# Performance work log

Hardware: AMD Instinct MI355X
Metric: run time of the kernel (lower is better)

Reference implementation:

```python
import jax, jax.numpy as jnp
import numpy as np

VOL = 64          # self.vol_size
SPACE = 0.2       # space_size (cubic), space_center = 0
IMG = 255.0       # normalization constant in the source (2*u/255 - 1)


def setup_inputs() -> dict:
    key = jax.random.key(0)
    ks = jax.random.split(key, 5)
    B, V, C, Hf, Wf = 2, 4, 32, 64, 64
    features = jax.random.normal(ks[0], (B, V, C, Hf, Wf), jnp.float32)
    # near-identity rotations, cameras ~0.5m away, focal ~200, principal point 128
    camera_R = jnp.eye(3, dtype=jnp.float32)[None, None] + 0.01 * jax.random.normal(ks[1], (B, V, 3, 3), jnp.float32)
    camera_T = jnp.array([0.0, 0.0, 0.5], jnp.float32) + 0.01 * jax.random.normal(ks[2], (B, V, 3), jnp.float32)
    K0 = jnp.array([[200.0, 0.0, 128.0], [0.0, 200.0, 128.0], [0.0, 0.0, 1.0]], jnp.float32)
    Kmask = jnp.array([[1.0, 0.0, 1.0], [0.0, 1.0, 1.0], [0.0, 0.0, 0.0]], jnp.float32)
    camera_K = K0[None, None] + 0.5 * jax.random.normal(ks[3], (B, V, 3, 3), jnp.float32) * Kmask
    root_world = 0.01 * jax.random.normal(ks[4], (B, 3), jnp.float32)
    return dict(features=features, camera_R=camera_R, camera_T=camera_T,
                camera_K=camera_K, root_world=root_world)


def _bilinear_sample(feat, x, y):
    """PyTorch F.grid_sample, mode=bilinear, padding=zeros, align_corners=False.
    feat: [N,C,H,W]; x,y: [N,P] pixel-space coords (already unnormalized).
    Returns [N,C,P]."""
    N, C, H, W = feat.shape
    x0 = jnp.floor(x); y0 = jnp.floor(y)
    x1 = x0 + 1.0;     y1 = y0 + 1.0
    wx1 = x - x0; wx0 = 1.0 - wx1
    wy1 = y - y0; wy0 = 1.0 - wy1
    feat_flat = feat.reshape(N, C, H * W)

    def gather(xi, yi, w):
        valid = (xi >= 0) & (xi <= W - 1) & (yi >= 0) & (yi <= H - 1)
        xi_c = jnp.clip(xi, 0, W - 1).astype(jnp.int32)
        yi_c = jnp.clip(yi, 0, H - 1).astype(jnp.int32)
        idx = yi_c * W + xi_c                                   # [N,P]
        vals = jnp.take_along_axis(feat_flat, idx[:, None, :], axis=2)  # [N,C,P]
        return vals * (w * valid.astype(feat.dtype))[:, None, :]

    return (gather(x0, y0, wx0 * wy0) + gather(x1, y0, wx1 * wy0)
            + gather(x0, y1, wx0 * wy1) + gather(x1, y1, wx1 * wy1))


def reference(features, camera_R, camera_T, camera_K, root_world):
    B, V, C, Hf, Wf = features.shape
    D = VOL
    # _build_grid: 64^3 points, xyz order, spanning SPACE around center 0
    r = jnp.arange(D, dtype=jnp.float32)
    z, y, x = jnp.meshgrid(r, r, r, indexing='ij')
    grid = jnp.stack([x, y, z], axis=0) / (D - 1)               # [3,D,D,D]
    pts = ((grid - 0.5) * SPACE).reshape(3, -1).T               # [P,3], P = D^3
    # relative camera translation: new_T = R @ root + T
    new_T = jnp.einsum('bvij,bj->bvi', camera_R, root_world) + camera_T
    # project: pts_cam = pts @ R^T + T  -> [B,V,P,3]
    pts_cam = jnp.einsum('pj,bvij->bvpi', pts, camera_R) + new_T[:, :, None, :]
    zc = jnp.maximum(pts_cam[..., 2], 1e-5)
    fx = camera_K[:, :, 0, 0][..., None]; fy = camera_K[:, :, 1, 1][..., None]
    cx = camera_K[:, :, 0, 2][..., None]; cy = camera_K[:, :, 1, 2][..., None]
    u = pts_cam[..., 0] * fx / zc + cx
    v = pts_cam[..., 1] * fy / zc + cy
    u_n = 2.0 * u / IMG - 1.0
    v_n = 2.0 * v / IMG - 1.0
    # unnormalize (align_corners=False): ix = ((g+1)*W - 1)/2
    px = ((u_n + 1.0) * Wf - 1.0) * 0.5
    py = ((v_n + 1.0) * Hf - 1.0) * 0.5
    feat_bv = features.reshape(B * V, C, Hf, Wf)
    vol = _bilinear_sample(feat_bv, px.reshape(B * V, -1), py.reshape(B * V, -1))  # [BV,C,P]
    vol = vol.reshape(B, V, C, D, D, D).mean(axis=1)            # average over views
    return vol
```

## Files before the change

### kernel.cpp

```cpp
#include <hip/hip_runtime.h>

#define B_   2
#define V_   4
#define C_   32
#define HW_  4096
#define D_   64
#define P_   (D_*D_*D_)
#define SCL_ (64.0f/255.0f)

typedef _Float16 half2v __attribute__((ext_vector_type(2)));

union Corner { uint4 u[2]; half2v h[8]; };

__global__ __launch_bounds__(256) void tx_kernel(const float* __restrict__ in,
                                                 unsigned int* __restrict__ out) {
    __shared__ float tile[32][65];
    const int bv  = blockIdx.x >> 6;
    const int hw0 = (blockIdx.x & 63) << 6;
    const int t   = threadIdx.x;
    const float* src = in + (size_t)bv * C_ * HW_ + hw0;
#pragma unroll
    for (int i = 0; i < 8; ++i) {
        int e = t + (i << 8);
        tile[e >> 6][e & 63] = src[(e >> 6) * HW_ + (e & 63)];
    }
    __syncthreads();
    unsigned int* dst = out + ((size_t)bv * HW_ + hw0) * (C_ / 2);
#pragma unroll
    for (int i = 0; i < 4; ++i) {
        int idx = t + (i << 8);
        int c  = (idx << 1) & 31;
        int hw = idx >> 4;
        half2v v = { (_Float16)tile[c][hw], (_Float16)tile[c + 1][hw] };
        dst[idx] = *(unsigned int*)&v;
    }
}

__global__ __launch_bounds__(256) void vol_kernel(
    const unsigned char* __restrict__ feat,
    const float* __restrict__ Rm,
    const float* __restrict__ Tm,
    const float* __restrict__ Km,
    const float* __restrict__ root,
    float* __restrict__ out)
{
    const int b = blockIdx.x >> 11;
    const int t = threadIdx.x;
    const int h = t & 1;
    const int p = ((blockIdx.x & 2047) << 7) | (t >> 1);
    const int xi = p & 63, yi = (p >> 6) & 63, zi = p >> 12;
    const float X = ((float)xi * (1.0f/63.0f) - 0.5f) * 0.2f;
    const float Y = ((float)yi * (1.0f/63.0f) - 0.5f) * 0.2f;
    const float Z = ((float)zi * (1.0f/63.0f) - 0.5f) * 0.2f;

    float acc[16];
#pragma unroll
    for (int j = 0; j < 16; ++j) acc[j] = 0.0f;

    const float rx = root[b*3+0], ry = root[b*3+1], rz = root[b*3+2];

#pragma unroll
    for (int v = 0; v < V_; ++v) {
        const int bv = b * V_ + v;
        const float* Rb = Rm + bv * 9;
        const float* Tb = Tm + bv * 3;
        const float* Kb = Km + bv * 9;
        const float r00=Rb[0], r01=Rb[1], r02=Rb[2];
        const float r10=Rb[3], r11=Rb[4], r12=Rb[5];
        const float r20=Rb[6], r21=Rb[7], r22=Rb[8];
        const float t0 = r00*rx + r01*ry + r02*rz + Tb[0];
        const float t1 = r10*rx + r11*ry + r12*rz + Tb[1];
        const float t2 = r20*rx + r21*ry + r22*rz + Tb[2];
        const float xc = r00*X + r01*Y + r02*Z + t0;
        const float yc = r10*X + r11*Y + r12*Z + t1;
        float zc       = r20*X + r21*Y + r22*Z + t2;
        zc = fmaxf(zc, 1e-5f);
        const float inv = 1.0f / zc;
        const float px = xc * (Kb[0]*SCL_) * inv + (Kb[2]*SCL_ - 0.5f);
        const float py = yc * (Kb[4]*SCL_) * inv + (Kb[5]*SCL_ - 0.5f);

        const float x0f = floorf(px), y0f = floorf(py);
        const float wx1 = px - x0f, wx0 = 1.0f - wx1;
        const float wy1 = py - y0f, wy0 = 1.0f - wy1;
        const float x1f = x0f + 1.0f, y1f = y0f + 1.0f;
        const float vx0 = (x0f >= 0.0f && x0f <= 63.0f) ? 1.0f : 0.0f;
        const float vx1 = (x1f >= 0.0f && x1f <= 63.0f) ? 1.0f : 0.0f;
        const float vy0 = (y0f >= 0.0f && y0f <= 63.0f) ? 1.0f : 0.0f;
        const float vy1 = (y1f >= 0.0f && y1f <= 63.0f) ? 1.0f : 0.0f;
        const float w00 = wx0*wy0*vx0*vy0*0.25f, w01 = wx1*wy0*vx1*vy0*0.25f;
        const float w10 = wx0*wy1*vx0*vy1*0.25f, w11 = wx1*wy1*vx1*vy1*0.25f;
        const int x0c = (int)fminf(fmaxf(x0f, 0.0f), 63.0f);
        const int x1c = (int)fminf(fmaxf(x1f, 0.0f), 63.0f);
        const int y0c = (int)fminf(fmaxf(y0f, 0.0f), 63.0f);
        const int y1c = (int)fminf(fmaxf(y1f, 0.0f), 63.0f);

        const unsigned char* fb = feat + (size_t)bv * HW_ * 64 + h * 32;
        const Corner c00 = *(const Corner*)(fb + (size_t)(y0c*64 + x0c) * 64);
        const Corner c01 = *(const Corner*)(fb + (size_t)(y0c*64 + x1c) * 64);
        const Corner c10 = *(const Corner*)(fb + (size_t)(y1c*64 + x0c) * 64);
        const Corner c11 = *(const Corner*)(fb + (size_t)(y1c*64 + x1c) * 64);

        const half2v w00h = { (_Float16)w00, (_Float16)w00 };
        const half2v w01h = { (_Float16)w01, (_Float16)w01 };
        const half2v w10h = { (_Float16)w10, (_Float16)w10 };
        const half2v w11h = { (_Float16)w11, (_Float16)w11 };
#pragma unroll
        for (int j = 0; j < 8; ++j) {
            half2v s = c00.h[j] * w00h;
            s += c01.h[j] * w01h;
            s += c10.h[j] * w10h;
            s += c11.h[j] * w11h;
            acc[2*j+0] += (float)s.x;
            acc[2*j+1] += (float)s.y;
        }
    }

    float* ob = out + ((size_t)(b * C_) + (h << 4)) * P_ + p;
#pragma unroll
    for (int j = 0; j < 16; ++j)
        __builtin_nontemporal_store(acc[j], ob + (size_t)j * P_);
}

__global__ __launch_bounds__(256) void vol_fallback(
    const float* __restrict__ feat,
    const float* __restrict__ Rm, const float* __restrict__ Tm,
    const float* __restrict__ Km, const float* __restrict__ root,
    float* __restrict__ out)
{
    const int b = blockIdx.x >> 10;
    const int p = ((blockIdx.x & 1023) << 8) | threadIdx.x;
    const int xi = p & 63, yi = (p >> 6) & 63, zi = p >> 12;
    const float X = ((float)xi * (1.0f/63.0f) - 0.5f) * 0.2f;
    const float Y = ((float)yi * (1.0f/63.0f) - 0.5f) * 0.2f;
    const float Z = ((float)zi * (1.0f/63.0f) - 0.5f) * 0.2f;
    float acc[C_];
#pragma unroll
    for (int c = 0; c < C_; ++c) acc[c] = 0.0f;
    const float rx = root[b*3+0], ry = root[b*3+1], rz = root[b*3+2];
#pragma unroll
    for (int v = 0; v < V_; ++v) {
        const int bv = b * V_ + v;
        const float* Rb = Rm + bv * 9; const float* Tb = Tm + bv * 3;
        const float* Kb = Km + bv * 9;
        const float r00=Rb[0], r01=Rb[1], r02=Rb[2];
        const float r10=Rb[3], r11=Rb[4], r12=Rb[5];
        const float r20=Rb[6], r21=Rb[7], r22=Rb[8];
        const float t0 = r00*rx + r01*ry + r02*rz + Tb[0];
        const float t1 = r10*rx + r11*ry + r12*rz + Tb[1];
        const float t2 = r20*rx + r21*ry + r22*rz + Tb[2];
        const float xc = r00*X + r01*Y + r02*Z + t0;
        const float yc = r10*X + r11*Y + r12*Z + t1;
        float zc       = r20*X + r21*Y + r22*Z + t2;
        zc = fmaxf(zc, 1e-5f);
        const float inv = 1.0f / zc;
        const float px = xc * (Kb[0]*SCL_) * inv + (Kb[2]*SCL_ - 0.5f);
        const float py = yc * (Kb[4]*SCL_) * inv + (Kb[5]*SCL_ - 0.5f);
        const float x0f = floorf(px), y0f = floorf(py);
        const float wx1 = px - x0f, wx0 = 1.0f - wx1;
        const float wy1 = py - y0f, wy0 = 1.0f - wy1;
        const float x1f = x0f + 1.0f, y1f = y0f + 1.0f;
        const float vx0 = (x0f >= 0.0f && x0f <= 63.0f) ? 1.0f : 0.0f;
        const float vx1 = (x1f >= 0.0f && x1f <= 63.0f) ? 1.0f : 0.0f;
        const float vy0 = (y0f >= 0.0f && y0f <= 63.0f) ? 1.0f : 0.0f;
        const float vy1 = (y1f >= 0.0f && y1f <= 63.0f) ? 1.0f : 0.0f;
        const float w00 = wx0*wy0*vx0*vy0, w01 = wx1*wy0*vx1*vy0;
        const float w10 = wx0*wy1*vx0*vy1, w11 = wx1*wy1*vx1*vy1;
        const int x0c = (int)fminf(fmaxf(x0f, 0.0f), 63.0f);
        const int x1c = (int)fminf(fmaxf(x1f, 0.0f), 63.0f);
        const int y0c = (int)fminf(fmaxf(y0f, 0.0f), 63.0f);
        const int y1c = (int)fminf(fmaxf(y1f, 0.0f), 63.0f);
        const float* fb = feat + (size_t)bv * C_ * HW_;
        const int i00 = y0c*64 + x0c, i01 = y0c*64 + x1c;
        const int i10 = y1c*64 + x0c, i11 = y1c*64 + x1c;
#pragma unroll
        for (int c = 0; c < C_; ++c) {
            const float* f = fb + c * HW_;
            acc[c] += w00*f[i00] + w01*f[i01] + w10*f[i10] + w11*f[i11];
        }
    }
    float* ob = out + (size_t)b * C_ * P_ + p;
#pragma unroll
    for (int c = 0; c < C_; ++c) ob[(size_t)c * P_] = acc[c] * 0.25f;
}

extern "C" void kernel_launch(void* const* d_in, const int* in_sizes, int n_in,
                              void* d_out, int out_size, void* d_ws, size_t ws_size,
                              hipStream_t stream) {
    const float* feat = (const float*)d_in[0];
    const float* Rm   = (const float*)d_in[1];
    const float* Tm   = (const float*)d_in[2];
    const float* Km   = (const float*)d_in[3];
    const float* root = (const float*)d_in[4];
    float* out = (float*)d_out;

    const size_t need = (size_t)B_ * V_ * HW_ * C_ * sizeof(_Float16);
    if (ws_size >= need) {
        unsigned int* ftx = (unsigned int*)d_ws;
        tx_kernel<<<B_ * V_ * 64, 256, 0, stream>>>(feat, ftx);
        vol_kernel<<<B_ * P_ / 128, 256, 0, stream>>>(
            (const unsigned char*)ftx, Rm, Tm, Km, root, out);
    } else {
        vol_fallback<<<B_ * P_ / 256, 256, 0, stream>>>(feat, Rm, Tm, Km, root, out);
    }
}
```

Before: 102.2 us.

## Split voxel work across 4 lanes, share projection via shuffles

Each voxel is now handled by 4 lanes instead of 2. Each lane computes the projection, bilinear weights and corner offsets for one view, then the lanes exchange them with warp shuffles, so the per-view projection math is no longer duplicated. Each lane loads 16-byte corner chunks and accumulates 8 channels, which doubles the block count and cuts registers per thread. Per-camera constants are precomputed once per block into shared memory. The cost is extra shuffle traffic, a block-level sync, and narrower gathers per lane.

Measured after the change: 102.0 us. Within noise of the previous version (-0.2%).

```diff
diff --git a/kernel.cpp b/kernel.cpp
--- a/kernel.cpp
+++ b/kernel.cpp
@@ -10,7 +10,7 @@
 
 typedef _Float16 half2v __attribute__((ext_vector_type(2)));
 
-union Corner { uint4 u[2]; half2v h[8]; };
+union Corner16 { uint4 u; half2v h[4]; };
 
 __global__ __launch_bounds__(256) void tx_kernel(const float* __restrict__ in,
                                                  unsigned int* __restrict__ out) {
@@ -44,80 +44,107 @@
     const float* __restrict__ root,
     float* __restrict__ out)
 {
-    const int b = blockIdx.x >> 11;
+    __shared__ __align__(16) float cam[4][20];
+
     const int t = threadIdx.x;
-    const int h = t & 1;
-    const int p = ((blockIdx.x & 2047) << 7) | (t >> 1);
+    const int q = t & 3;
+    const int b = blockIdx.x >> 12;
+    const int p = ((blockIdx.x & 4095) << 6) | (t >> 2);
+
+    if (t < 4) {
+        const int bv = b * V_ + t;
+        const float* Rb = Rm + bv * 9;
+        const float* Tb = Tm + bv * 3;
+        const float* Kb = Km + bv * 9;
+        const float rx = root[b*3+0], ry = root[b*3+1], rz = root[b*3+2];
+        cam[t][0] = Rb[0]; cam[t][1] = Rb[1]; cam[t][2] = Rb[2];
+        cam[t][3] = Rb[0]*rx + Rb[1]*ry + Rb[2]*rz + Tb[0];
+        cam[t][4] = Rb[3]; cam[t][5] = Rb[4]; cam[t][6] = Rb[5];
+        cam[t][7] = Rb[3]*rx + Rb[4]*ry + Rb[5]*rz + Tb[1];
+        cam[t][8] = Rb[6]; cam[t][9] = Rb[7]; cam[t][10] = Rb[8];
+        cam[t][11] = Rb[6]*rx + Rb[7]*ry + Rb[8]*rz + Tb[2];
+        cam[t][12] = Kb[0] * SCL_;
+        cam[t][13] = Kb[4] * SCL_;
+        cam[t][14] = Kb[2] * SCL_ - 0.5f;
+        cam[t][15] = Kb[5] * SCL_ - 0.5f;
+    }
+    __syncthreads();
+
     const int xi = p & 63, yi = (p >> 6) & 63, zi = p >> 12;
     const float X = ((float)xi * (1.0f/63.0f) - 0.5f) * 0.2f;
     const float Y = ((float)yi * (1.0f/63.0f) - 0.5f) * 0.2f;
     const float Z = ((float)zi * (1.0f/63.0f) - 0.5f) * 0.2f;
 
-    float acc[16];
-#pragma unroll
-    for (int j = 0; j < 16; ++j) acc[j] = 0.0f;
-
-    const float rx = root[b*3+0], ry = root[b*3+1], rz = root[b*3+2];
+    const float4 cA = *(const float4*)&cam[q][0];
+    const float4 cB = *(const float4*)&cam[q][4];
+    const float4 cC = *(const float4*)&cam[q][8];
+    const float4 cK = *(const float4*)&cam[q][12];
+    const float xc = cA.x*X + cA.y*Y + cA.z*Z + cA.w;
+    const float yc = cB.x*X + cB.y*Y + cB.z*Z + cB.w;
+    float zc       = cC.x*X + cC.y*Y + cC.z*Z + cC.w;
+    zc = fmaxf(zc, 1e-5f);
+    const float inv = 1.0f / zc;
+    const float px = (xc * inv) * cK.x + cK.z;
+    const float py = (yc * inv) * cK.y + cK.w;
+
+    const float x0f = floorf(px), y0f = floorf(py);
+    const float wx1 = px - x0f, wx0 = 1.0f - wx1;
+    const float wy1 = py - y0f, wy0 = 1.0f - wy1;
+    const float x1f = x0f + 1.0f, y1f = y0f + 1.0f;
+    const float vx0 = (x0f >= 0.0f && x0f <= 63.0f) ? 1.0f : 0.0f;
+    const float vx1 = (x1f >= 0.0f && x1f <= 63.0f) ? 1.0f : 0.0f;
+    const float vy0 = (y0f >= 0.0f && y0f <= 63.0f) ? 1.0f : 0.0f;
+    const float vy1 = (y1f >= 0.0f && y1f <= 63.0f) ? 1.0f : 0.0f;
+    const float w00 = wx0*wy0*vx0*vy0*0.25f, w01 = wx1*wy0*vx1*vy0*0.25f;
+    const float w10 = wx0*wy1*vx0*vy1*0.25f, w11 = wx1*wy1*vx1*vy1*0.25f;
+    const int x0c = (int)fminf(fmaxf(x0f, 0.0f), 63.0f);
+    const int x1c = (int)fminf(fmaxf(x1f, 0.0f), 63.0f);
+    const int y0c = (int)fminf(fmaxf(y0f, 0.0f), 63.0f);
+    const int y1c = (int)fminf(fmaxf(y1f, 0.0f), 63.0f);
+    const int bvbase = (b * V_ + q) * HW_;
+    const int o00 = (bvbase + y0c*64 + x0c) << 6;
+    const int o01 = (bvbase + y0c*64 + x1c) << 6;
+    const int o10 = (bvbase + y1c*64 + x0c) << 6;
+    const int o11 = (bvbase + y1c*64 + x1c) << 6;
+
+    float acc[8];
+#pragma unroll
+    for (int j = 0; j < 8; ++j) acc[j] = 0.0f;
+
+    const unsigned char* fb = feat + (q << 4);
+    const int lane_base = t & ~3;
 
 #pragma unroll
     for (int v = 0; v < V_; ++v) {
-        const int bv = b * V_ + v;
-        const float* Rb = Rm + bv * 9;
-        const float* Tb = Tm + bv * 3;
-        const float* Kb = Km + bv * 9;
-        const float r00=Rb[0], r01=Rb[1], r02=Rb[2];
-        const float r10=Rb[3], r11=Rb[4], r12=Rb[5];
-        const float r20=Rb[6], r21=Rb[7], r22=Rb[8];
-        const float t0 = r00*rx + r01*ry + r02*rz + Tb[0];
-        const float t1 = r10*rx + r11*ry + r12*rz + Tb[1];
-        const float t2 = r20*rx + r21*ry + r22*rz + Tb[2];
-        const float xc = r00*X + r01*Y + r02*Z + t0;
-        const float yc = r10*X + r11*Y + r12*Z + t1;
-        float zc       = r20*X + r21*Y + r22*Z + t2;
-        zc = fmaxf(zc, 1e-5f);
-        const float inv = 1.0f / zc;
-        const float px = xc * (Kb[0]*SCL_) * inv + (Kb[2]*SCL_ - 0.5f);
-        const float py = yc * (Kb[4]*SCL_) * inv + (Kb[5]*SCL_ - 0.5f);
-
-        const float x0f = floorf(px), y0f = floorf(py);
-        const float wx1 = px - x0f, wx0 = 1.0f - wx1;
-        const float wy1 = py - y0f, wy0 = 1.0f - wy1;
-        const float x1f = x0f + 1.0f, y1f = y0f + 1.0f;
-        const float vx0 = (x0f >= 0.0f && x0f <= 63.0f) ? 1.0f : 0.0f;
-        const float vx1 = (x1f >= 0.0f && x1f <= 63.0f) ? 1.0f : 0.0f;
-        const float vy0 = (y0f >= 0.0f && y0f <= 63.0f) ? 1.0f : 0.0f;
-        const float vy1 = (y1f >= 0.0f && y1f <= 63.0f) ? 1.0f : 0.0f;
-        const float w00 = wx0*wy0*vx0*vy0*0.25f, w01 = wx1*wy0*vx1*vy0*0.25f;
-        const float w10 = wx0*wy1*vx0*vy1*0.25f, w11 = wx1*wy1*vx1*vy1*0.25f;
-        const int x0c = (int)fminf(fmaxf(x0f, 0.0f), 63.0f);
-        const int x1c = (int)fminf(fmaxf(x1f, 0.0f), 63.0f);
-        const int y0c = (int)fminf(fmaxf(y0f, 0.0f), 63.0f);
-        const int y1c = (int)fminf(fmaxf(y1f, 0.0f), 63.0f);
-
-        const unsigned char* fb = feat + (size_t)bv * HW_ * 64 + h * 32;
-        const Corner c00 = *(const Corner*)(fb + (size_t)(y0c*64 + x0c) * 64);
-        const Corner c01 = *(const Corner*)(fb + (size_t)(y0c*64 + x1c) * 64);
-        const Corner c10 = *(const Corner*)(fb + (size_t)(y1c*64 + x0c) * 64);
-        const Corner c11 = *(const Corner*)(fb + (size_t)(y1c*64 + x1c) * 64);
-
-        const half2v w00h = { (_Float16)w00, (_Float16)w00 };
-        const half2v w01h = { (_Float16)w01, (_Float16)w01 };
-        const half2v w10h = { (_Float16)w10, (_Float16)w10 };
-        const half2v w11h = { (_Float16)w11, (_Float16)w11 };
-#pragma unroll
-        for (int j = 0; j < 8; ++j) {
-            half2v s = c00.h[j] * w00h;
-            s += c01.h[j] * w01h;
-            s += c10.h[j] * w10h;
-            s += c11.h[j] * w11h;
+        const int src = lane_base | v;
+        const float sw00 = __shfl(w00, src), sw01 = __shfl(w01, src);
+        const float sw10 = __shfl(w10, src), sw11 = __shfl(w11, src);
+        const int so00 = __shfl(o00, src), so01 = __shfl(o01, src);
+        const int so10 = __shfl(o10, src), so11 = __shfl(o11, src);
+
+        const Corner16 c00 = *(const Corner16*)(fb + (size_t)(unsigned)so00);
+        const Corner16 c01 = *(const Corner16*)(fb + (size_t)(unsigned)so01);
+        const Corner16 c10 = *(const Corner16*)(fb + (size_t)(unsigned)so10);
+        const Corner16 c11 = *(const Corner16*)(fb + (size_t)(unsigned)so11);
+
+        const half2v h00 = { (_Float16)sw00, (_Float16)sw00 };
+        const half2v h01 = { (_Float16)sw01, (_Float16)sw01 };
+        const half2v h10 = { (_Float16)sw10, (_Float16)sw10 };
+        const half2v h11 = { (_Float16)sw11, (_Float16)sw11 };
+#pragma unroll
+        for (int j = 0; j < 4; ++j) {
+            half2v s = c00.h[j] * h00;
+            s += c01.h[j] * h01;
+            s += c10.h[j] * h10;
+            s += c11.h[j] * h11;
             acc[2*j+0] += (float)s.x;
             acc[2*j+1] += (float)s.y;
         }
     }
 
-    float* ob = out + ((size_t)(b * C_) + (h << 4)) * P_ + p;
-#pragma unroll
-    for (int j = 0; j < 16; ++j)
+    float* ob = out + ((size_t)(b * C_) + (q << 3)) * P_ + p;
+#pragma unroll
+    for (int j = 0; j < 8; ++j)
         __builtin_nontemporal_store(acc[j], ob + (size_t)j * P_);
 }
 
@@ -197,7 +224,7 @@
     if (ws_size >= need) {
         unsigned int* ftx = (unsigned int*)d_ws;
         tx_kernel<<<B_ * V_ * 64, 256, 0, stream>>>(feat, ftx);
-        vol_kernel<<<B_ * P_ / 128, 256, 0, stream>>>(
+        vol_kernel<<<B_ * P_ / 64, 256, 0, stream>>>(
             (const unsigned char*)ftx, Rm, Tm, Km, root, out);
     } else {
         vol_fallback<<<B_ * P_ / 256, 256, 0, stream>>>(feat, Rm, Tm, Km, root, out);
```
